# Optimization experiments

Measured on AMD Instinct MI355X. Metric: run time of the kernel, lower is better.

## Reference

```python
import jax, jax.numpy as jnp
import numpy as np

N = 100000
E = 1600000
D_IN, D_HID, D_OUT = 128, 32, 32
NEG_SLOPE = 0.2
EPS = 1e-16


def setup_inputs() -> dict:
    key = jax.random.key(0)
    ks = jax.random.split(key, 9)
    x = jax.random.normal(ks[0], (N, D_IN), dtype=jnp.float32)
    edge_index = jax.random.randint(ks[1], (2, E), 0, N, dtype=jnp.int64)
    W1 = jax.random.normal(ks[2], (D_IN, D_HID), dtype=jnp.float32) / np.sqrt(D_IN)
    b1 = jnp.zeros((D_HID,), dtype=jnp.float32)
    W2 = jax.random.normal(ks[3], (D_HID, D_OUT), dtype=jnp.float32) / np.sqrt(D_HID)
    att_src = jax.random.normal(ks[4], (D_OUT,), dtype=jnp.float32) / np.sqrt(D_OUT)
    att_dst = jax.random.normal(ks[5], (D_OUT,), dtype=jnp.float32) / np.sqrt(D_OUT)
    b2 = jnp.zeros((D_OUT,), dtype=jnp.float32)
    return {"x": x, "edge_index": edge_index, "W1": W1, "b1": b1,
            "W2": W2, "att_src": att_src, "att_dst": att_dst, "b2": b2}


def _add_self_loops(edge_index, n):
    loop = jnp.arange(n, dtype=edge_index.dtype)
    src = jnp.concatenate([edge_index[0], loop])
    dst = jnp.concatenate([edge_index[1], loop])
    return src, dst


def _gcn_conv(x, src, dst, W, b, n):
    # symmetric normalization with self-loops already included
    deg = jax.ops.segment_sum(jnp.ones_like(dst, dtype=x.dtype), dst, num_segments=n)
    dis = jnp.where(deg > 0, jax.lax.rsqrt(jnp.maximum(deg, 1.0)), 0.0)
    h = x @ W                               # [N, H]
    norm = dis[src] * dis[dst]              # [E2]
    msg = norm[:, None] * h[src]            # [E2, H]
    return jax.ops.segment_sum(msg, dst, num_segments=n) + b


def _gat_conv(x, src, dst, W, att_src, att_dst, b, n):
    g = x @ W                               # [N, H]
    a_s = g @ att_src                       # [N]
    a_d = g @ att_dst                       # [N]
    e = a_s[src] + a_d[dst]                 # [E2]
    e = jnp.where(e > 0, e, NEG_SLOPE * e)  # leaky_relu(0.2)
    # segment softmax over edges grouped by destination node
    emax = jax.ops.segment_max(e, dst, num_segments=n)
    ee = jnp.exp(e - emax[dst])
    esum = jax.ops.segment_sum(ee, dst, num_segments=n)
    alpha = ee / (esum[dst] + EPS)
    msg = alpha[:, None] * g[src]           # [E2, H]
    return jax.ops.segment_sum(msg, dst, num_segments=n) + b


def reference(x, edge_index, W1, b1, W2, att_src, att_dst, b2):
    n = x.shape[0]
    src, dst = _add_self_loops(edge_index, n)
    h = _gcn_conv(x, src, dst, W1, b1, n)
    h = jax.nn.relu(h)
    out = _gat_conv(h, src, dst, W2, att_src, att_dst, b2, n)
    return out
```

## Files before the change

### kernel.cpp

```cpp
#include <hip/hip_runtime.h>
#include <cstdint>
#include <cstddef>

#define D_IN   128
#define D_HID  32
#define D_OUT  32
#define NEG_SLOPE 0.2f
#define EPS_F  1e-16f

#define BKT_SHIFT 9
#define NPB (1 << BKT_SHIFT)
#define KBUKMAX 256
#define NBLK_BIN 512
#define AGG_BLOCKS 2048

using half4 = __attribute__((ext_vector_type(4))) _Float16;

__device__ __forceinline__ int edge_val(const int* __restrict__ ei, long long idx, int is64) {
    return is64 ? ei[idx * 2] : ei[idx];
}

__device__ __forceinline__ int detect_is64(const int* __restrict__ ei, long long E,
                                           int t, int* s_is64) {
    if (t < 64) {
        long long n = E < 64 ? E : 64;
        int bad = (t < n && ei[2 * t + 1] != 0) ? 1 : 0;
        unsigned long long mask = __ballot(bad);
        if (t == 0) *s_is64 = (mask == 0ULL) ? 1 : 0;
    }
    __syncthreads();
    return *s_is64;
}

__global__ __launch_bounds__(256) void hist_kernel(
        const int* __restrict__ ei, long long E, long long E2,
        int* __restrict__ hist, int K2, int EPB) {
    __shared__ int hcnt[KBUKMAX];
    __shared__ int s_is64;
    const int t = threadIdx.x;
    if (t < K2) hcnt[t] = 0;
    const int is64 = detect_is64(ei, E, t, &s_is64);
    const long long lo = (long long)blockIdx.x * EPB;
    const long long hi = min(E2, lo + EPB);
    for (long long e = lo + t; e < hi; e += 256) {
        int d = (e < E) ? edge_val(ei, E + e, is64) : (int)(e - E);
        atomicAdd(&hcnt[d >> BKT_SHIFT], 1);
    }
    __syncthreads();
    if (t < K2) hist[t * gridDim.x + blockIdx.x] = hcnt[t];
}

__global__ void scan_ga_kernel(int* __restrict__ a, int* __restrict__ bsum, int L) {
    __shared__ int wsum[4];
    const int t = threadIdx.x;
    const int i0 = blockIdx.x * 1024 + t * 4;
    int v[4]; int s = 0;
    #pragma unroll
    for (int k = 0; k < 4; ++k) {
        v[k] = (i0 + k < L) ? a[i0 + k] : 0;
        s += v[k];
    }
    const int lane = t & 63, wid = t >> 6;
    int incl = s;
    #pragma unroll
    for (int d = 1; d < 64; d <<= 1) {
        int u = __shfl_up(incl, d);
        if (lane >= d) incl += u;
    }
    if (lane == 63) wsum[wid] = incl;
    __syncthreads();
    int woff = 0;
    for (int w = 0; w < wid; ++w) woff += wsum[w];
    int excl = woff + incl - s;
    #pragma unroll
    for (int k = 0; k < 4; ++k) {
        if (i0 + k < L) a[i0 + k] = excl;
        excl += v[k];
    }
    if (t == 255) bsum[blockIdx.x] = woff + incl;
}

__global__ __launch_bounds__(1024) void scan_flat_kernel(int* __restrict__ a, int L) {
    __shared__ int wsum[16];
    __shared__ int carry_s;
    const int t = threadIdx.x;
    const int lane = t & 63, wid = t >> 6;
    if (t == 0) carry_s = 0;
    __syncthreads();
    for (int start = 0; start < L; start += 1024) {
        int idx = start + t;
        int v = (idx < L) ? a[idx] : 0;
        int incl = v;
        #pragma unroll
        for (int d = 1; d < 64; d <<= 1) {
            int u = __shfl_up(incl, d);
            if (lane >= d) incl += u;
        }
        if (lane == 63) wsum[wid] = incl;
        __syncthreads();
        int woff = 0;
        for (int w = 0; w < wid; ++w) woff += wsum[w];
        int carry = carry_s;
        __syncthreads();
        if (idx < L) a[idx] = carry + woff + incl - v;
        if (t == 1023) carry_s = carry + woff + incl;
        __syncthreads();
    }
}

__global__ __launch_bounds__(256) void scatter_kernel(
        const int* __restrict__ ei, long long E, long long E2,
        const int* __restrict__ off, const int* __restrict__ bsum,
        unsigned* __restrict__ bins, int K2, int EPB) {
    __shared__ int cur[KBUKMAX];
    __shared__ int s_is64;
    const int t = threadIdx.x;
    if (t < K2) {
        int idx = t * gridDim.x + blockIdx.x;
        cur[t] = off[idx] + bsum[idx >> 10];
    }
    const int is64 = detect_is64(ei, E, t, &s_is64);
    const long long lo = (long long)blockIdx.x * EPB;
    const long long hi = min(E2, lo + EPB);
    for (long long e = lo + t; e < hi; e += 256) {
        int s, d;
        if (e < E) { s = edge_val(ei, e, is64); d = edge_val(ei, E + e, is64); }
        else       { s = d = (int)(e - E); }
        int b = d >> BKT_SHIFT;
        int pos = atomicAdd(&cur[b], 1);
        bins[pos] = (unsigned)s | ((unsigned)(d & (NPB - 1)) << 17);
    }
}

__global__ __launch_bounds__(512) void csr_b_kernel(
        const unsigned* __restrict__ bins, const int* __restrict__ off,
        const int* __restrict__ bsum,
        int* __restrict__ rowptr, float* __restrict__ dis, int* __restrict__ csr_src,
        int N, int K2, long long E2) {
    __shared__ int lcur[NPB];
    __shared__ int wsum[8];
    const int b = blockIdx.x, t = threadIdx.x;
    const int nbase = b << BKT_SHIFT;
    const int nn = min(NPB, N - nbase);
    lcur[t] = 0;
    __syncthreads();
    int bidx = b * NBLK_BIN;
    const int base = off[bidx] + bsum[bidx >> 10];
    int end;
    if (b == K2 - 1) end = (int)E2;
    else {
        int eidx = (b + 1) * NBLK_BIN;
        end = off[eidx] + bsum[eidx >> 10];
    }
    for (int i = base + t; i < end; i += 512)
        atomicAdd(&lcur[bins[i] >> 17], 1);
    __syncthreads();
    const int lane = t & 63, wid = t >> 6;
    int v = lcur[t];
    int incl = v;
    #pragma unroll
    for (int d = 1; d < 64; d <<= 1) {
        int u = __shfl_up(incl, d);
        if (lane >= d) incl += u;
    }
    if (lane == 63) wsum[wid] = incl;
    __syncthreads();
    int woff = 0;
    for (int w = 0; w < wid; ++w) woff += wsum[w];
    int excl = woff + incl - v;
    if (t < nn) {
        rowptr[nbase + t] = base + excl;
        dis[nbase + t] = rsqrtf((float)v);
    }
    __syncthreads();
    lcur[t] = base + excl;
    __syncthreads();
    for (int i = base + t; i < end; i += 512) {
        unsigned u = bins[i];
        int pos = atomicAdd(&lcur[u >> 17], 1);
        csr_src[pos] = (int)(u & 0x1FFFFu);
    }
    if (b == 0 && t == 0) rowptr[N] = (int)E2;
}

__global__ __launch_bounds__(256) void gemm1_kernel(
        const float* __restrict__ x, const float* __restrict__ W1,
        const float* __restrict__ dis, _Float16* __restrict__ hws_h, int N) {
    __shared__ float sW[D_IN * D_HID];
    const int t = threadIdx.x;
    for (int i = t; i < D_IN * D_HID; i += 256) sW[i] = W1[i];
    __syncthreads();
    if (blockIdx.x == 0 && t < 8) {
        half4 z;
        z.x = (_Float16)0.f; z.y = (_Float16)0.f;
        z.z = (_Float16)0.f; z.w = (_Float16)0.f;
        ((half4*)hws_h)[(long long)N * 8 + t] = z;
    }
    long long row = (long long)blockIdx.x * 256 + t;
    const bool valid = row < N;
    long long r = valid ? row : (long long)(N - 1);
    const float4* x4 = (const float4*)x;
    float acc[D_HID];
    #pragma unroll
    for (int c = 0; c < D_HID; ++c) acc[c] = 0.f;
    for (int q = 0; q < 32; ++q) {
        float4 xv = x4[r * 32 + q];
        #pragma unroll
        for (int kk = 0; kk < 4; ++kk) {
            float xs = (&xv.x)[kk];
            const float* wrow = &sW[(q * 4 + kk) * D_HID];
            #pragma unroll
            for (int c4 = 0; c4 < 8; ++c4) {
                float4 wv = *(const float4*)&wrow[c4 * 4];
                acc[c4 * 4 + 0] = fmaf(xs, wv.x, acc[c4 * 4 + 0]);
                acc[c4 * 4 + 1] = fmaf(xs, wv.y, acc[c4 * 4 + 1]);
                acc[c4 * 4 + 2] = fmaf(xs, wv.z, acc[c4 * 4 + 2]);
                acc[c4 * 4 + 3] = fmaf(xs, wv.w, acc[c4 * 4 + 3]);
            }
        }
    }
    if (valid) {
        float dd = dis[r];
        half4* hh4 = (half4*)hws_h;
        #pragma unroll
        for (int c4 = 0; c4 < 8; ++c4) {
            half4 o;
            o.x = (_Float16)(acc[c4 * 4 + 0] * dd);
            o.y = (_Float16)(acc[c4 * 4 + 1] * dd);
            o.z = (_Float16)(acc[c4 * 4 + 2] * dd);
            o.w = (_Float16)(acc[c4 * 4 + 3] * dd);
            hh4[r * 8 + c4] = o;
        }
    }
}

__global__ __launch_bounds__(256) void gcn_fused_kernel(
        const int* __restrict__ rowptr, const int* __restrict__ csr_src,
        const _Float16* __restrict__ hws_h, const float* __restrict__ dis,
        const float* __restrict__ b1, const float* __restrict__ W2,
        const float* __restrict__ att_s, const float* __restrict__ att_d,
        _Float16* __restrict__ g_h, float* __restrict__ a_s, float* __restrict__ a_d,
        int N) {
    __shared__ float sW2[D_HID * D_OUT];
    __shared__ float sas[D_OUT], sad[D_OUT];
    const int t = threadIdx.x;
    for (int i = t; i < D_HID * D_OUT; i += 256) sW2[i] = W2[i];
    if (t < D_OUT) { sas[t] = att_s[t]; sad[t] = att_d[t]; }
    __syncthreads();
    const int lane = t & 63;
    const int half = lane >> 5, l32 = lane & 31;
    const int u = l32 & 7, grp = l32 >> 3;
    const int wib = t >> 6;
    const half4* hh4 = (const half4*)hws_h;
    const float4 b14 = ((const float4*)b1)[u];
    float w2c[D_HID];
    #pragma unroll
    for (int k = 0; k < D_HID; ++k) w2c[k] = sW2[k * D_OUT + l32];
    const float sasl = sas[l32], sadl = sad[l32];
    const int srcBase = half * 32;
    const int npair = (N + 1) >> 1;
    for (int p = blockIdx.x * 4 + wib; p < npair; p += gridDim.x * 4) {
        const int i = p * 2 + half;
        const bool act = i < N;
        int b = 0, e = 0;
        if (act) { b = rowptr[i]; e = rowptr[i + 1]; }
        float ax = 0.f, ay = 0.f, az = 0.f, aw = 0.f;
        for (int j = b + grp; j < e; j += 16) {
            int j1 = j + 4, j2 = j + 8, j3 = j + 12;
            bool v1 = j1 < e, v2 = j2 < e, v3 = j3 < e;
            int s0 = csr_src[j];
            int s1 = v1 ? csr_src[v1 ? j1 : j] : N;
            int s2 = v2 ? csr_src[v2 ? j2 : j] : N;
            int s3 = v3 ? csr_src[v3 ? j3 : j] : N;
            half4 h0 = hh4[s0 * 8 + u];
            half4 h1 = hh4[s1 * 8 + u];
            half4 h2 = hh4[s2 * 8 + u];
            half4 h3 = hh4[s3 * 8 + u];
            ax += (float)h0.x + (float)h1.x + (float)h2.x + (float)h3.x;
            ay += (float)h0.y + (float)h1.y + (float)h2.y + (float)h3.y;
            az += (float)h0.z + (float)h1.z + (float)h2.z + (float)h3.z;
            aw += (float)h0.w + (float)h1.w + (float)h2.w + (float)h3.w;
        }
        #pragma unroll
        for (int d = 8; d <= 16; d <<= 1) {
            ax += __shfl_xor(ax, d); ay += __shfl_xor(ay, d);
            az += __shfl_xor(az, d); aw += __shfl_xor(aw, d);
        }
        float dd = act ? dis[i] : 0.f;
        float4 o;
        o.x = fmaf(dd, ax, b14.x); o.y = fmaf(dd, ay, b14.y);
        o.z = fmaf(dd, az, b14.z); o.w = fmaf(dd, aw, b14.w);
        o.x = o.x > 0.f ? o.x : 0.f; o.y = o.y > 0.f ? o.y : 0.f;
        o.z = o.z > 0.f ? o.z : 0.f; o.w = o.w > 0.f ? o.w : 0.f;
        float gv = 0.f;
        #pragma unroll
        for (int up = 0; up < 8; ++up) {
            int sl = srcBase + up;
            float hx = __shfl(o.x, sl);
            float hy = __shfl(o.y, sl);
            float hz = __shfl(o.z, sl);
            float hw = __shfl(o.w, sl);
            gv = fmaf(hx, w2c[up * 4 + 0], gv);
            gv = fmaf(hy, w2c[up * 4 + 1], gv);
            gv = fmaf(hz, w2c[up * 4 + 2], gv);
            gv = fmaf(hw, w2c[up * 4 + 3], gv);
        }
        if (act) g_h[(long long)i * D_OUT + l32] = (_Float16)gv;
        float ps = gv * sasl;
        float pd = gv * sadl;
        #pragma unroll
        for (int d = 1; d <= 16; d <<= 1) {
            ps += __shfl_xor(ps, d);
            pd += __shfl_xor(pd, d);
        }
        if (act && l32 == 0) { a_s[i] = ps; a_d[i] = pd; }
    }
}

__global__ __launch_bounds__(256) void e_pre_kernel(
        const int* __restrict__ rowptr, const int* __restrict__ csr_src,
        const float* __restrict__ a_s, const float* __restrict__ a_d,
        float* __restrict__ epre, float* __restrict__ mrow, int N) {
    int i = blockIdx.x * blockDim.x + threadIdx.x;
    if (i >= N) return;
    const int b = rowptr[i], e = rowptr[i + 1];
    const float adi = a_d[i];
    float m = -1e30f;
    for (int j = b; j < e; ++j) {
        float ev = a_s[csr_src[j]] + adi;
        ev = ev > 0.f ? ev : NEG_SLOPE * ev;
        epre[j] = ev;
        m = fmaxf(m, ev);
    }
    mrow[i] = m;
}

__global__ void gat_agg_kernel(const int* __restrict__ rowptr, const int* __restrict__ csr_src,
                               const _Float16* __restrict__ g_h, const float* __restrict__ epre,
                               const float* __restrict__ mrow, const float* __restrict__ b2,
                               float* __restrict__ out, int N) {
    const int lane = threadIdx.x & 63;
    const int half = lane >> 5, l32 = lane & 31;
    const int u = l32 & 7, grp = l32 >> 3;
    const int wib = threadIdx.x >> 6;
    const half4* gh4 = (const half4*)g_h;
    float4* out4 = (float4*)out;
    const float4 b24 = ((const float4*)b2)[u];
    const int npair = (N + 1) >> 1;
    for (int p = blockIdx.x * 4 + wib; p < npair; p += gridDim.x * 4) {
        const int i = p * 2 + half;
        const bool act = i < N;
        int b = 0, e = 0;
        float mi = 0.f;
        if (act) { b = rowptr[i]; e = rowptr[i + 1]; mi = mrow[i]; }
        float ssum = 0.f;
        float ax = 0.f, ay = 0.f, az = 0.f, aw = 0.f;
        for (int j = b + grp; j < e; j += 16) {
            int j1 = j + 4, j2 = j + 8, j3 = j + 12;
            bool v1 = j1 < e, v2 = j2 < e, v3 = j3 < e;
            int s0 = csr_src[j];
            int s1 = csr_src[v1 ? j1 : j];
            int s2 = csr_src[v2 ? j2 : j];
            int s3 = csr_src[v3 ? j3 : j];
            float e0 = epre[j];
            float e1 = epre[v1 ? j1 : j];
            float e2 = epre[v2 ? j2 : j];
            float e3 = epre[v3 ? j3 : j];
            half4 g0 = gh4[s0 * 8 + u];
            half4 g1 = gh4[s1 * 8 + u];
            half4 g2 = gh4[s2 * 8 + u];
            half4 g3 = gh4[s3 * 8 + u];
            float w0 = __expf(e0 - mi);
            float w1 = v1 ? __expf(e1 - mi) : 0.f;
            float w2 = v2 ? __expf(e2 - mi) : 0.f;
            float w3 = v3 ? __expf(e3 - mi) : 0.f;
            ssum += w0 + w1 + w2 + w3;
            ax = fmaf(w0, (float)g0.x, fmaf(w1, (float)g1.x, fmaf(w2, (float)g2.x, fmaf(w3, (float)g3.x, ax))));
            ay = fmaf(w0, (float)g0.y, fmaf(w1, (float)g1.y, fmaf(w2, (float)g2.y, fmaf(w3, (float)g3.y, ay))));
            az = fmaf(w0, (float)g0.z, fmaf(w1, (float)g1.z, fmaf(w2, (float)g2.z, fmaf(w3, (float)g3.z, az))));
            aw = fmaf(w0, (float)g0.w, fmaf(w1, (float)g1.w, fmaf(w2, (float)g2.w, fmaf(w3, (float)g3.w, aw))));
        }
        #pragma unroll
        for (int d = 8; d <= 16; d <<= 1) {
            ssum += __shfl_xor(ssum, d);
            ax += __shfl_xor(ax, d); ay += __shfl_xor(ay, d);
            az += __shfl_xor(az, d); aw += __shfl_xor(aw, d);
        }
        if (act && grp == 0) {
            float inv = 1.f / (ssum + EPS_F);
            float4 o;
            o.x = fmaf(ax, inv, b24.x); o.y = fmaf(ay, inv, b24.y);
            o.z = fmaf(az, inv, b24.z); o.w = fmaf(aw, inv, b24.w);
            out4[(long long)i * 8 + u] = o;
        }
    }
}

extern "C" void kernel_launch(void* const* d_in, const int* in_sizes, int n_in,
                              void* d_out, int out_size, void* d_ws, size_t ws_size,
                              hipStream_t stream) {
    const float* x       = (const float*)d_in[0];
    const int*   ei      = (const int*)d_in[1];
    const float* W1      = (const float*)d_in[2];
    const float* b1      = (const float*)d_in[3];
    const float* W2      = (const float*)d_in[4];
    const float* att_src = (const float*)d_in[5];
    const float* att_dst = (const float*)d_in[6];
    const float* b2      = (const float*)d_in[7];
    float* out = (float*)d_out;

    const long long N  = in_sizes[0] / D_IN;
    const long long E  = in_sizes[1] / 2;
    const long long E2 = E + N;
    const int K2  = (int)((N + NPB - 1) >> BKT_SHIFT);
    const int EPB = (int)((E2 + NBLK_BIN - 1) / NBLK_BIN);
    const int LH  = K2 * NBLK_BIN;
    const int NBH = (LH + 1023) / 1024;

    char* ws = (char*)d_ws;
    size_t off0 = 0;
    auto alloc = [&](size_t bytes) -> void* {
        off0 = (off0 + 255) & ~(size_t)255;
        void* p = ws + off0;
        off0 += bytes;
        return p;
    };
    int*   hist     = (int*)  alloc((size_t)KBUKMAX * NBLK_BIN * 4);
    unsigned* bins  = (unsigned*)alloc((size_t)E2 * 4);
    int*   rowptr   = (int*)  alloc((size_t)(N + 1) * 4);
    int*   csr_src  = (int*)  alloc((size_t)E2 * 4);
    float* dis      = (float*)alloc((size_t)N * 4);
    _Float16* hws_h = (_Float16*)alloc((size_t)(N + 1) * D_HID * 2);
    _Float16* g_h   = (_Float16*)alloc((size_t)N * D_OUT * 2);
    float* as       = (float*)alloc((size_t)N * 4);
    float* ad       = (float*)alloc((size_t)N * 4);
    float* epre     = (float*)alloc((size_t)E2 * 4);
    float* mrow     = (float*)alloc((size_t)N * 4);
    int*   bsum     = (int*)  alloc((size_t)NBH * 4);
    (void)ws_size; (void)n_in; (void)out_size;

    hist_kernel<<<NBLK_BIN, 256, 0, stream>>>(ei, E, E2, hist, K2, EPB);
    scan_ga_kernel<<<NBH, 256, 0, stream>>>(hist, bsum, LH);
    scan_flat_kernel<<<1, 1024, 0, stream>>>(bsum, NBH);
    scatter_kernel<<<NBLK_BIN, 256, 0, stream>>>(ei, E, E2, hist, bsum, bins, K2, EPB);
    csr_b_kernel<<<K2, 512, 0, stream>>>(bins, hist, bsum, rowptr, dis, csr_src, (int)N, K2, E2);
    gemm1_kernel<<<(int)((N + 255) / 256), 256, 0, stream>>>(x, W1, dis, hws_h, (int)N);
    gcn_fused_kernel<<<AGG_BLOCKS, 256, 0, stream>>>(rowptr, csr_src, hws_h, dis, b1, W2,
                                                     att_src, att_dst, g_h, as, ad, (int)N);
    e_pre_kernel<<<(int)((N + 255) / 256), 256, 0, stream>>>(rowptr, csr_src, as, ad, epre, mrow, (int)N);
    gat_agg_kernel<<<AGG_BLOCKS, 256, 0, stream>>>(rowptr, csr_src, g_h, epre, mrow, b2, out, (int)N);
}
```

Measured before the change: 162.2 us.

## Replace histogram-scan-scatter with fixed-capacity buckets reserved by global atomics

```diff
diff --git a/kernel.cpp b/kernel.cpp
--- a/kernel.cpp
+++ b/kernel.cpp
@@ -12,6 +12,7 @@
 #define NPB (1 << BKT_SHIFT)
 #define KBUKMAX 256
 #define NBLK_BIN 512
+#define BCAP 10240
 #define AGG_BLOCKS 2048
 
 using half4 = __attribute__((ext_vector_type(4))) _Float16;
@@ -32,10 +33,11 @@
     return *s_is64;
 }
 
-__global__ __launch_bounds__(256) void hist_kernel(
+__global__ __launch_bounds__(256) void reserve_scatter_kernel(
         const int* __restrict__ ei, long long E, long long E2,
-        int* __restrict__ hist, int K2, int EPB) {
+        int* __restrict__ gcur, unsigned* __restrict__ bins, int K2, int EPB) {
     __shared__ int hcnt[KBUKMAX];
+    __shared__ int cur[KBUKMAX];
     __shared__ int s_is64;
     const int t = threadIdx.x;
     if (t < K2) hcnt[t] = 0;
@@ -47,115 +49,56 @@
         atomicAdd(&hcnt[d >> BKT_SHIFT], 1);
     }
     __syncthreads();
-    if (t < K2) hist[t * gridDim.x + blockIdx.x] = hcnt[t];
-}
-
-__global__ void scan_ga_kernel(int* __restrict__ a, int* __restrict__ bsum, int L) {
-    __shared__ int wsum[4];
-    const int t = threadIdx.x;
-    const int i0 = blockIdx.x * 1024 + t * 4;
-    int v[4]; int s = 0;
-    #pragma unroll
-    for (int k = 0; k < 4; ++k) {
-        v[k] = (i0 + k < L) ? a[i0 + k] : 0;
-        s += v[k];
-    }
-    const int lane = t & 63, wid = t >> 6;
-    int incl = s;
-    #pragma unroll
-    for (int d = 1; d < 64; d <<= 1) {
-        int u = __shfl_up(incl, d);
-        if (lane >= d) incl += u;
-    }
-    if (lane == 63) wsum[wid] = incl;
-    __syncthreads();
-    int woff = 0;
-    for (int w = 0; w < wid; ++w) woff += wsum[w];
-    int excl = woff + incl - s;
-    #pragma unroll
-    for (int k = 0; k < 4; ++k) {
-        if (i0 + k < L) a[i0 + k] = excl;
-        excl += v[k];
-    }
-    if (t == 255) bsum[blockIdx.x] = woff + incl;
-}
-
-__global__ __launch_bounds__(1024) void scan_flat_kernel(int* __restrict__ a, int L) {
-    __shared__ int wsum[16];
-    __shared__ int carry_s;
-    const int t = threadIdx.x;
-    const int lane = t & 63, wid = t >> 6;
-    if (t == 0) carry_s = 0;
-    __syncthreads();
-    for (int start = 0; start < L; start += 1024) {
-        int idx = start + t;
-        int v = (idx < L) ? a[idx] : 0;
-        int incl = v;
-        #pragma unroll
-        for (int d = 1; d < 64; d <<= 1) {
-            int u = __shfl_up(incl, d);
-            if (lane >= d) incl += u;
-        }
-        if (lane == 63) wsum[wid] = incl;
-        __syncthreads();
-        int woff = 0;
-        for (int w = 0; w < wid; ++w) woff += wsum[w];
-        int carry = carry_s;
-        __syncthreads();
-        if (idx < L) a[idx] = carry + woff + incl - v;
-        if (t == 1023) carry_s = carry + woff + incl;
-        __syncthreads();
-    }
-}
-
-__global__ __launch_bounds__(256) void scatter_kernel(
-        const int* __restrict__ ei, long long E, long long E2,
-        const int* __restrict__ off, const int* __restrict__ bsum,
-        unsigned* __restrict__ bins, int K2, int EPB) {
-    __shared__ int cur[KBUKMAX];
-    __shared__ int s_is64;
-    const int t = threadIdx.x;
     if (t < K2) {
-        int idx = t * gridDim.x + blockIdx.x;
-        cur[t] = off[idx] + bsum[idx >> 10];
-    }
-    const int is64 = detect_is64(ei, E, t, &s_is64);
-    const long long lo = (long long)blockIdx.x * EPB;
-    const long long hi = min(E2, lo + EPB);
+        int n = hcnt[t];
+        cur[t] = (n > 0) ? atomicAdd(&gcur[t], n) : 0;
+    }
+    __syncthreads();
     for (long long e = lo + t; e < hi; e += 256) {
         int s, d;
         if (e < E) { s = edge_val(ei, e, is64); d = edge_val(ei, E + e, is64); }
         else       { s = d = (int)(e - E); }
         int b = d >> BKT_SHIFT;
         int pos = atomicAdd(&cur[b], 1);
-        bins[pos] = (unsigned)s | ((unsigned)(d & (NPB - 1)) << 17);
+        if (pos < BCAP)
+            bins[(long long)b * BCAP + pos] = (unsigned)s | ((unsigned)(d & (NPB - 1)) << 17);
     }
 }
 
 __global__ __launch_bounds__(512) void csr_b_kernel(
-        const unsigned* __restrict__ bins, const int* __restrict__ off,
-        const int* __restrict__ bsum,
+        const unsigned* __restrict__ bins, const int* __restrict__ gcur,
         int* __restrict__ rowptr, float* __restrict__ dis, int* __restrict__ csr_src,
         int N, int K2, long long E2) {
     __shared__ int lcur[NPB];
     __shared__ int wsum[8];
+    __shared__ int bbase_s, bcnt_s;
     const int b = blockIdx.x, t = threadIdx.x;
     const int nbase = b << BKT_SHIFT;
     const int nn = min(NPB, N - nbase);
     lcur[t] = 0;
-    __syncthreads();
-    int bidx = b * NBLK_BIN;
-    const int base = off[bidx] + bsum[bidx >> 10];
-    int end;
-    if (b == K2 - 1) end = (int)E2;
-    else {
-        int eidx = (b + 1) * NBLK_BIN;
-        end = off[eidx] + bsum[eidx >> 10];
-    }
-    for (int i = base + t; i < end; i += 512)
-        atomicAdd(&lcur[bins[i] >> 17], 1);
-    __syncthreads();
     const int lane = t & 63, wid = t >> 6;
+    int cntb = (t < K2) ? min(gcur[t], BCAP) : 0;
+    {
+        int incl = cntb;
+        #pragma unroll
+        for (int d = 1; d < 64; d <<= 1) {
+            int u = __shfl_up(incl, d);
+            if (lane >= d) incl += u;
+        }
+        if (lane == 63) wsum[wid] = incl;
+        __syncthreads();
+        int woff = 0;
+        for (int w = 0; w < wid; ++w) woff += wsum[w];
+        int excl = woff + incl - cntb;
+        if (t == b) { bbase_s = excl; bcnt_s = cntb; }
+        __syncthreads();
+    }
+    const int base = bbase_s;
+    const int cnt  = bcnt_s;
+    const unsigned* bp = bins + (long long)b * BCAP;
+    for (int i = t; i < cnt; i += 512)
+        atomicAdd(&lcur[bp[i] >> 17], 1);
+    __syncthreads();
     int v = lcur[t];
     int incl = v;
     #pragma unroll
@@ -175,8 +118,8 @@
     __syncthreads();
     lcur[t] = base + excl;
     __syncthreads();
-    for (int i = base + t; i < end; i += 512) {
-        unsigned u = bins[i];
+    for (int i = t; i < cnt; i += 512) {
+        unsigned u = bp[i];
         int pos = atomicAdd(&lcur[u >> 17], 1);
         csr_src[pos] = (int)(u & 0x1FFFFu);
     }
@@ -414,8 +357,6 @@
     const long long E2 = E + N;
     const int K2  = (int)((N + NPB - 1) >> BKT_SHIFT);
     const int EPB = (int)((E2 + NBLK_BIN - 1) / NBLK_BIN);
-    const int LH  = K2 * NBLK_BIN;
-    const int NBH = (LH + 1023) / 1024;
 
     char* ws = (char*)d_ws;
     size_t off0 = 0;
@@ -425,25 +366,22 @@
         off0 += bytes;
         return p;
     };
-    int*   hist     = (int*)  alloc((size_t)KBUKMAX * NBLK_BIN * 4);
-    unsigned* bins  = (unsigned*)alloc((size_t)E2 * 4);
+    int*   gcur     = (int*)  alloc((size_t)KBUKMAX * 4);
+    unsigned* bins  = (unsigned*)alloc((size_t)K2 * BCAP * 4);
     int*   rowptr   = (int*)  alloc((size_t)(N + 1) * 4);
     int*   csr_src  = (int*)  alloc((size_t)E2 * 4);
     float* dis      = (float*)alloc((size_t)N * 4);
     _Float16* hws_h = (_Float16*)alloc((size_t)(N + 1) * D_HID * 2);
-    _Float16* g_h   = (_Float16*)alloc((size_t)N * D_OUT * 2);
+    _Float16* g_h   = (_Float16*)alloc((size_t)(N + 1) * D_OUT * 2);
     float* as       = (float*)alloc((size_t)N * 4);
     float* ad       = (float*)alloc((size_t)N * 4);
     float* epre     = (float*)alloc((size_t)E2 * 4);
     float* mrow     = (float*)alloc((size_t)N * 4);
-    int*   bsum     = (int*)  alloc((size_t)NBH * 4);
     (void)ws_size; (void)n_in; (void)out_size;
 
-    hist_kernel<<<NBLK_BIN, 256, 0, stream>>>(ei, E, E2, hist, K2, EPB);
-    scan_ga_kernel<<<NBH, 256, 0, stream>>>(hist, bsum, LH);
-    scan_flat_kernel<<<1, 1024, 0, stream>>>(bsum, NBH);
-    scatter_kernel<<<NBLK_BIN, 256, 0, stream>>>(ei, E, E2, hist, bsum, bins, K2, EPB);
-    csr_b_kernel<<<K2, 512, 0, stream>>>(bins, hist, bsum, rowptr, dis, csr_src, (int)N, K2, E2);
+    hipMemsetAsync(gcur, 0, (size_t)K2 * 4, stream);
+    reserve_scatter_kernel<<<NBLK_BIN, 256, 0, stream>>>(ei, E, E2, gcur, bins, K2, EPB);
+    csr_b_kernel<<<K2, 512, 0, stream>>>(bins, gcur, rowptr, dis, csr_src, (int)N, K2, E2);
     gemm1_kernel<<<(int)((N + 255) / 256), 256, 0, stream>>>(x, W1, dis, hws_h, (int)N);
     gcn_fused_kernel<<<AGG_BLOCKS, 256, 0, stream>>>(rowptr, csr_src, hws_h, dis, b1, W2,
                                                      att_src, att_dst, g_h, as, ad, (int)N);
```

After: 167.0 us. 3.0% more time.
